# Performance work log

Measured on AMD Instinct MI355X. Metric: run time of the kernel, lower is better.

The kernel has to match this reference:

```python
import jax, jax.numpy as jnp
import numpy as np

NUM_REL = 3


def setup_inputs() -> dict:
    key = jax.random.key(0)
    ks = jax.random.split(key, 12)
    N, E, G = 400_000, 2_000_000, 40_000
    V, D, H, C = 1024, 64, 96, 8
    sc = lambda k, shape: (jax.random.normal(k, shape, jnp.float32) * 0.05)
    return {
        "tokens": jax.random.randint(ks[0], (N,), 0, V),
        "edge_index": jax.random.randint(ks[1], (2, E), 0, N),
        "edge_type": jax.random.randint(ks[2], (E,), 0, NUM_REL),
        "batch": jnp.sort(jax.random.randint(ks[3], (N,), 0, G)),
        "num_graphs": G,
        "emb": sc(ks[4], (V, D)),
        "W1": sc(ks[5], (NUM_REL, D, H)),
        "root1": sc(ks[6], (D, H)),
        "b1": jnp.zeros((H,), jnp.float32),
        "W2": sc(ks[7], (NUM_REL, H, H)),
        "root2": sc(ks[8], (H, H)),
        "b2": jnp.zeros((H,), jnp.float32),
        "linW": sc(ks[9], (H, C)),
        "linb": jnp.zeros((C,), jnp.float32),
    }


def rgcn_layer(x, src, dst, etype, W, root, bias):
    # PyG RGCNConv with default aggr='mean': per-relation mean over incoming
    # edges, transformed by the relation weight, plus root transform and bias.
    N, Din = x.shape
    seg = dst * NUM_REL + etype  # combined (node, relation) segment id
    msgs = x[src]  # [E, Din] irregular gather
    sums = jax.ops.segment_sum(msgs, seg, num_segments=N * NUM_REL)
    sums = sums.reshape(N, NUM_REL, Din)
    cnt = jax.ops.segment_sum(jnp.ones_like(etype, dtype=x.dtype), seg,
                              num_segments=N * NUM_REL).reshape(N, NUM_REL, 1)
    mean = sums / jnp.maximum(cnt, 1.0)
    return jnp.einsum("nrd,rdh->nh", mean, W) + x @ root + bias


def reference(tokens, edge_index, edge_type, batch, num_graphs,
              emb, W1, root1, b1, W2, root2, b2, linW, linb):
    src, dst = edge_index[0], edge_index[1]
    x = emb[tokens]  # [N, D]
    x = jax.nn.relu(rgcn_layer(x, src, dst, edge_type, W1, root1, b1))
    # dropout(p=0.2) is identity in eval mode
    x = jax.nn.relu(rgcn_layer(x, src, dst, edge_type, W2, root2, b2))
    gsum = jax.ops.segment_sum(x, batch, num_segments=num_graphs)
    gcnt = jax.ops.segment_sum(jnp.ones((x.shape[0], 1), x.dtype), batch,
                               num_segments=num_graphs)
    pooled = gsum / jnp.maximum(gcnt, 1.0)  # global_mean_pool
    return pooled @ linW + linb
```

## Files before the change

kernel.cpp:

```cpp
#include <hip/hip_runtime.h>


#define NREL 3
#define DD 64
#define HH 96
#define CC 8
#define TM 16
#define KK 384

typedef __attribute__((ext_vector_type(8))) short bf16x8;
typedef __attribute__((ext_vector_type(4))) short s16x4;
typedef __attribute__((ext_vector_type(4))) float f32x4;

__device__ __forceinline__ unsigned short f2bf(float x) {
    unsigned u = __float_as_uint(x);
    unsigned r = (u + 0x7fffu + ((u >> 16) & 1u)) >> 16;
    return (unsigned short)r;
}
__device__ __forceinline__ float bf2f(unsigned short h) {
    return __uint_as_float(((unsigned)h) << 16);
}

__global__ __launch_bounds__(256) void count_k(const int* __restrict__ dstv,
                                               const int* __restrict__ et, int E,
                                               int* __restrict__ cnt) {
    int e = blockIdx.x * 256 + threadIdx.x;
    if (e < E) atomicAdd(&cnt[dstv[e] * NREL + et[e]], 1);
}

__global__ __launch_bounds__(256) void scan_blk_k(const int* __restrict__ in, int S,
                                                  int* __restrict__ out,
                                                  int* __restrict__ bsum) {
    __shared__ int vals[1024];
    __shared__ int tsum[256];
    int base = blockIdx.x * 1024;
    for (int i = threadIdx.x; i < 1024; i += 256) {
        int g = base + i;
        vals[i] = (g < S) ? in[g] : 0;
    }
    __syncthreads();
    int t = threadIdx.x;
    int a0 = vals[t * 4], a1 = vals[t * 4 + 1], a2 = vals[t * 4 + 2], a3 = vals[t * 4 + 3];
    int s = a0 + a1 + a2 + a3;
    tsum[t] = s;
    __syncthreads();
    for (int off = 1; off < 256; off <<= 1) {
        int v = (t >= off) ? tsum[t - off] : 0;
        __syncthreads();
        tsum[t] += v;
        __syncthreads();
    }
    int excl = tsum[t] - s;
    int g = base + t * 4;
    if (g     < S) out[g]     = excl;
    if (g + 1 < S) out[g + 1] = excl + a0;
    if (g + 2 < S) out[g + 2] = excl + a0 + a1;
    if (g + 3 < S) out[g + 3] = excl + a0 + a1 + a2;
    if (t == 255) bsum[blockIdx.x] = tsum[255];
}

__global__ __launch_bounds__(256) void scan_top_k(int* __restrict__ bsum, int nb) {
    __shared__ int ts[256];
    int t = threadIdx.x;
    int loc[8];
    int s = 0;
    #pragma unroll
    for (int j = 0; j < 8; ++j) {
        int g = t * 8 + j;
        loc[j] = (g < nb) ? bsum[g] : 0;
        s += loc[j];
    }
    ts[t] = s;
    __syncthreads();
    for (int off = 1; off < 256; off <<= 1) {
        int v = (t >= off) ? ts[t - off] : 0;
        __syncthreads();
        ts[t] += v;
        __syncthreads();
    }
    int excl = ts[t] - s;
    #pragma unroll
    for (int j = 0; j < 8; ++j) {
        int g = t * 8 + j;
        if (g < nb) bsum[g] = excl;
        excl += loc[j];
    }
}

__global__ __launch_bounds__(256) void scan_add_k(int* __restrict__ out,
                                                  const int* __restrict__ bsum,
                                                  int S, int E) {
    int i = blockIdx.x * 256 + threadIdx.x;
    if (i < S) out[i] += bsum[i >> 10];
    else if (i == S) out[S] = E;
}

__global__ __launch_bounds__(256) void copy_k(const int* __restrict__ a,
                                              int* __restrict__ b, int n) {
    int i = blockIdx.x * 256 + threadIdx.x;
    if (i < n) b[i] = a[i];
}

__global__ __launch_bounds__(256) void fill_k(const int* __restrict__ srcv,
                                              const int* __restrict__ dstv,
                                              const int* __restrict__ et,
                                              const int* __restrict__ tokens, int E,
                                              int* __restrict__ cursor,
                                              int* __restrict__ ssrc,
                                              int* __restrict__ stok) {
    int e = blockIdx.x * 256 + threadIdx.x;
    if (e >= E) return;
    int s = srcv[e];
    int seg = dstv[e] * NREL + et[e];
    int pos = atomicAdd(&cursor[seg], 1);
    ssrc[pos] = s;
    stok[pos] = tokens[s];
}

__global__ __launch_bounds__(256) void gcnt_k(const int* __restrict__ batch, int N,
                                              float* __restrict__ gcnt) {
    int i = blockIdx.x * 256 + threadIdx.x;
    if (i < N) atomicAdd(&gcnt[batch[i]], 1.0f);
}

__global__ __launch_bounds__(256) void z1er_k(const float* __restrict__ emb,
                                              const float* __restrict__ W1,
                                              const float* __restrict__ root1,
                                              const float* __restrict__ b1,
                                              int V, float* __restrict__ z1,
                                              float* __restrict__ er1) {
    int idx = blockIdx.x * 256 + threadIdx.x;
    int tot = V * 4 * HH;
    if (idx >= tot) return;
    int v = idx / (4 * HH);
    int j = idx - v * 4 * HH;
    int r = j / HH;
    int h = j - r * HH;
    const float* ev = emb + (size_t)v * DD;
    float s = 0.f;
    if (r < NREL) {
        const float* w = W1 + ((size_t)r * DD) * HH + h;
        #pragma unroll 8
        for (int d = 0; d < DD; ++d) s += ev[d] * w[(size_t)d * HH];
        z1[((size_t)v * NREL + r) * HH + h] = s;
    } else {
        const float* w = root1 + h;
        #pragma unroll 8
        for (int d = 0; d < DD; ++d) s += ev[d] * w[(size_t)d * HH];
        er1[(size_t)v * HH + h] = s + b1[h];
    }
}

__global__ __launch_bounds__(256) void catwT_k(const float* __restrict__ W2,
                                               const float* __restrict__ root2,
                                               short* __restrict__ WTh,
                                               short* __restrict__ WTl) {
    int idx = blockIdx.x * 256 + threadIdx.x;
    const int tot = HH * KK;
    if (idx >= tot) return;
    int h = idx / KK;
    int K = idx - h * KK;
    float v = (K < NREL * HH) ? W2[(size_t)K * HH + h]
                              : root2[(size_t)(K - NREL * HH) * HH + h];
    unsigned short hi = f2bf(v);
    float res = v - bf2f(hi);
    unsigned short lo = f2bf(res);
    WTh[(size_t)h * KK + K] = (short)hi;
    WTl[(size_t)h * KK + K] = (short)lo;
}

__global__ __launch_bounds__(256) void l1_k(const int* __restrict__ rowptr,
                                            const int* __restrict__ stok,
                                            const int* __restrict__ tokens,
                                            const float* __restrict__ z1,
                                            const float* __restrict__ er1,
                                            unsigned short* __restrict__ h1h, int N) {
    int idx = blockIdx.x * 256 + threadIdx.x;
    if (idx >= N * 24) return;
    int n = idx / 24;
    int q = idx - n * 24;
    int h0 = q * 4;
    float4 acc = *reinterpret_cast<const float4*>(er1 + (size_t)tokens[n] * HH + h0);
    int base = n * NREL;
    for (int r = 0; r < NREL; ++r) {
        int b = rowptr[base + r], e2 = rowptr[base + r + 1];
        float sx = 0.f, sy = 0.f, sz = 0.f, sw = 0.f;
        for (int i = b; i < e2; i += 4) {
            int m = e2 - i;
            int t0 = stok[i];
            int t1 = stok[i + (m > 1 ? 1 : 0)];
            int t2 = stok[i + (m > 2 ? 2 : 0)];
            int t3 = stok[i + (m > 3 ? 3 : 0)];
            const float4 z0 = *reinterpret_cast<const float4*>(
                z1 + ((size_t)t0 * NREL + r) * HH + h0);
            const float4 zv1 = *reinterpret_cast<const float4*>(
                z1 + ((size_t)t1 * NREL + r) * HH + h0);
            const float4 zv2 = *reinterpret_cast<const float4*>(
                z1 + ((size_t)t2 * NREL + r) * HH + h0);
            const float4 zv3 = *reinterpret_cast<const float4*>(
                z1 + ((size_t)t3 * NREL + r) * HH + h0);
            float w1 = m > 1 ? 1.f : 0.f;
            float w2 = m > 2 ? 1.f : 0.f;
            float w3 = m > 3 ? 1.f : 0.f;
            sx += z0.x + zv1.x * w1 + zv2.x * w2 + zv3.x * w3;
            sy += z0.y + zv1.y * w1 + zv2.y * w2 + zv3.y * w3;
            sz += z0.z + zv1.z * w1 + zv2.z * w2 + zv3.z * w3;
            sw += z0.w + zv1.w * w1 + zv2.w * w2 + zv3.w * w3;
        }
        float rc = 1.0f / fmaxf((float)(e2 - b), 1.0f);
        acc.x += sx * rc; acc.y += sy * rc; acc.z += sz * rc; acc.w += sw * rc;
    }
    s16x4 hv;
    hv[0] = (short)f2bf(fmaxf(acc.x, 0.f));
    hv[1] = (short)f2bf(fmaxf(acc.y, 0.f));
    hv[2] = (short)f2bf(fmaxf(acc.z, 0.f));
    hv[3] = (short)f2bf(fmaxf(acc.w, 0.f));
    *reinterpret_cast<s16x4*>(&h1h[(size_t)n * HH + h0]) = hv;
}

__global__ __launch_bounds__(256) void quant_k(const unsigned short* __restrict__ h1h,
                                               unsigned* __restrict__ h1q, int N) {
    int idx = blockIdx.x * 256 + threadIdx.x;
    int n = idx >> 4;
    int l = idx & 15;
    if (n >= N) return;
    const unsigned* row = reinterpret_cast<const unsigned*>(h1h + (size_t)n * HH) + 3 * l;
    unsigned u0 = row[0], u1 = row[1], u2 = row[2];
    float v[6] = { bf2f((unsigned short)(u0 & 0xffff)), bf2f((unsigned short)(u0 >> 16)),
                   bf2f((unsigned short)(u1 & 0xffff)), bf2f((unsigned short)(u1 >> 16)),
                   bf2f((unsigned short)(u2 & 0xffff)), bf2f((unsigned short)(u2 >> 16)) };
    float m = 0.f;
    #pragma unroll
    for (int j = 0; j < 6; ++j) m = fmaxf(m, v[j]);
    #pragma unroll
    for (int mask = 1; mask <= 8; mask <<= 1) m = fmaxf(m, __shfl_xor(m, mask));
    unsigned eb = __float_as_uint(m) >> 23;
    unsigned E8;
    float qs;
    if (eb < 40) {
        E8 = 0; qs = 0.f;
    } else {
        E8 = eb - 9;
        qs = __uint_as_float((263 - eb) << 23);
    }
    unsigned q[6];
    #pragma unroll
    for (int j = 0; j < 6; ++j) {
        unsigned qi = (unsigned)__float2int_rn(v[j] * qs);
        q[j] = qi > 1023u ? 1023u : qi;
    }
    int d0 = 2 * l;
    unsigned e0 = (E8 >> (2 * (d0 & 3))) & 3u;
    unsigned e1 = (E8 >> (2 * ((d0 + 1) & 3))) & 3u;
    uint2 w;
    w.x = q[0] | (q[1] << 10) | (q[2] << 20) | (e0 << 30);
    w.y = q[3] | (q[4] << 10) | (q[5] << 20) | (e1 << 30);
    *reinterpret_cast<uint2*>(h1q + (size_t)n * 32 + d0) = w;
}

__device__ __forceinline__ float scof(const uint4& c) {
    unsigned E8 = (c.x >> 30) | ((c.y >> 30) << 2) | ((c.z >> 30) << 4)
                | ((c.w >> 30) << 6);
    return __uint_as_float(E8 << 23);
}
__device__ __forceinline__ void dec12(const uint4& c, float sc, float* acc) {
    acc[0]  += (float)(c.x & 1023u) * sc;
    acc[1]  += (float)((c.x >> 10) & 1023u) * sc;
    acc[2]  += (float)((c.x >> 20) & 1023u) * sc;
    acc[3]  += (float)(c.y & 1023u) * sc;
    acc[4]  += (float)((c.y >> 10) & 1023u) * sc;
    acc[5]  += (float)((c.y >> 20) & 1023u) * sc;
    acc[6]  += (float)(c.z & 1023u) * sc;
    acc[7]  += (float)((c.z >> 10) & 1023u) * sc;
    acc[8]  += (float)((c.z >> 20) & 1023u) * sc;
    acc[9]  += (float)(c.w & 1023u) * sc;
    acc[10] += (float)((c.w >> 10) & 1023u) * sc;
    acc[11] += (float)((c.w >> 20) & 1023u) * sc;
}

__global__ __launch_bounds__(384, 7) void l2_k(const int* __restrict__ rowptr,
                                               const int* __restrict__ ssrc,
                                               const unsigned* __restrict__ h1q,
                                               const unsigned short* __restrict__ h1h,
                                               const short* __restrict__ WTh,
                                               const short* __restrict__ WTl,
                                               const float* __restrict__ b2,
                                               const int* __restrict__ batch,
                                               float* __restrict__ gsum, int N) {
    __shared__ float Af32[TM][392];
    __shared__ int rp[49];
    short* ab = (short*)&Af32[0][0];
    int n0 = blockIdx.x * TM;
    int t = threadIdx.x;
    if (t < 49) {
        int idx = n0 * NREL + t;
        int mx = N * NREL;
        rp[t] = rowptr[idx < mx ? idx : mx];
    }
    __syncthreads();
    {
        int grp = t >> 3, l = t & 7;
        int i = grp & 15, r = grp >> 4;
        int n = n0 + i;
        if (n < N) {
            int b = rp[i * NREL + r], e2 = rp[i * NREL + r + 1];
            float acc[12];
            #pragma unroll
            for (int j = 0; j < 12; ++j) acc[j] = 0.f;
            for (int ge = b; ge < e2; ge += 4) {
                int m = e2 - ge;
                int s0 = ssrc[ge];
                int s1 = ssrc[ge + (m > 1 ? 1 : 0)];
                int s2 = ssrc[ge + (m > 2 ? 2 : 0)];
                int s3 = ssrc[ge + (m > 3 ? 3 : 0)];
                uint4 c0 = *reinterpret_cast<const uint4*>(h1q + (size_t)s0 * 32 + 4 * l);
                uint4 c1 = *reinterpret_cast<const uint4*>(h1q + (size_t)s1 * 32 + 4 * l);
                uint4 c2 = *reinterpret_cast<const uint4*>(h1q + (size_t)s2 * 32 + 4 * l);
                uint4 c3 = *reinterpret_cast<const uint4*>(h1q + (size_t)s3 * 32 + 4 * l);
                float f0 = scof(c0);
                float f1 = m > 1 ? scof(c1) : 0.f;
                float f2 = m > 2 ? scof(c2) : 0.f;
                float f3 = m > 3 ? scof(c3) : 0.f;
                dec12(c0, f0, acc);
                dec12(c1, f1, acc);
                dec12(c2, f2, acc);
                dec12(c3, f3, acc);
            }
            float rc = 1.0f / fmaxf((float)(e2 - b), 1.0f);
            #pragma unroll
            for (int j = 0; j < 12; j += 4) {
                float4 v = {acc[j] * rc, acc[j + 1] * rc, acc[j + 2] * rc,
                            acc[j + 3] * rc};
                *reinterpret_cast<float4*>(&Af32[i][r * HH + 12 * l + j]) = v;
            }
        }
    }
    __syncthreads();
    int i2 = t & 15;
    int c2 = t >> 4;
    int d0 = c2 * 16;
    int n2 = n0 + i2;
    float a[16];
    #pragma unroll
    for (int j = 0; j < 16; ++j) a[j] = 0.f;
    if (n2 < N) {
        if (c2 < 18) {
            #pragma unroll
            for (int j = 0; j < 16; ++j) a[j] = Af32[i2][d0 + j];
        } else {
            int k0 = (c2 - 18) * 16;
            const unsigned short* hr = h1h + (size_t)n2 * HH + k0;
            bf16x8 v0 = *reinterpret_cast<const bf16x8*>(hr);
            bf16x8 v1 = *reinterpret_cast<const bf16x8*>(hr + 8);
            #pragma unroll
            for (int j = 0; j < 8; ++j) {
                a[j]     = bf2f((unsigned short)v0[j]);
                a[8 + j] = bf2f((unsigned short)v1[j]);
            }
        }
    }
    __syncthreads();
    {
        bf16x8 hv, lv;
        #pragma unroll
        for (int w = 0; w < 2; ++w) {
            #pragma unroll
            for (int jj = 0; jj < 8; ++jj) {
                float x = a[w * 8 + jj];
                unsigned short hb = f2bf(x);
                float res = x - bf2f(hb);
                hv[jj] = (short)hb;
                lv[jj] = (short)f2bf(res);
            }
            *reinterpret_cast<bf16x8*>(ab + i2 * 392 + d0 + w * 8) = hv;
            *reinterpret_cast<bf16x8*>(ab + TM * 392 + i2 * 392 + d0 + w * 8) = lv;
        }
    }
    __syncthreads();
    int lane = t & 63;
    int w = t >> 6;
    int nb_ = w * 16;
    int r16 = lane & 15;
    int g = lane >> 4;

    float bi = b2[nb_ + r16];
    f32x4 acc = {bi, bi, bi, bi};

    const short* arow_h = ab + r16 * 392 + 8 * g;
    const short* arow_l = ab + TM * 392 + r16 * 392 + 8 * g;
    size_t wb = (size_t)(nb_ + r16) * KK + 8 * g;

    #pragma unroll
    for (int kk = 0; kk < KK / 32; ++kk) {
        int ko = kk * 32;
        bf16x8 ah = *reinterpret_cast<const bf16x8*>(arow_h + ko);
        bf16x8 al = *reinterpret_cast<const bf16x8*>(arow_l + ko);
        bf16x8 bh = *reinterpret_cast<const bf16x8*>(WTh + wb + ko);
        bf16x8 bl = *reinterpret_cast<const bf16x8*>(WTl + wb + ko);
        acc = __builtin_amdgcn_mfma_f32_16x16x32_bf16(ah, bh, acc, 0, 0, 0);
        acc = __builtin_amdgcn_mfma_f32_16x16x32_bf16(al, bh, acc, 0, 0, 0);
        acc = __builtin_amdgcn_mfma_f32_16x16x32_bf16(ah, bl, acc, 0, 0, 0);
    }
    #pragma unroll
    for (int r = 0; r < 4; ++r) {
        int node = n0 + g * 4 + r;
        if (node < N) {
            atomicAdd(gsum + (size_t)batch[node] * HH + nb_ + r16, fmaxf(acc[r], 0.f));
        }
    }
}

__global__ __launch_bounds__(256) void final_k(const float* __restrict__ gsum,
                                               const float* __restrict__ gcnt,
                                               const float* __restrict__ linW,
                                               const float* __restrict__ linb,
                                               float* __restrict__ out, int G) {
    int idx = blockIdx.x * 256 + threadIdx.x;
    if (idx >= G * CC) return;
    int g = idx / CC;
    int c = idx - g * CC;
    float rc = 1.0f / fmaxf(gcnt[g], 1.0f);
    const float* gs = gsum + (size_t)g * HH;
    float s = 0.f;
    #pragma unroll 8
    for (int h = 0; h < HH; ++h) s += gs[h] * linW[h * CC + c];
    out[idx] = s * rc + linb[c];
}

__global__ __launch_bounds__(256) void diag_k(float* __restrict__ out, int n, float v) {
    int i = blockIdx.x * 256 + threadIdx.x;
    if (i < n) out[i] = (i == 0) ? v : 0.f;
}

static inline int nblk(long long n) { return (int)((n + 255) / 256); }

extern "C" void kernel_launch(void* const* d_in, const int* in_sizes, int n_in,
                              void* d_out, int out_size, void* d_ws, size_t ws_size,
                              hipStream_t stream) {
    (void)n_in;
    const int* tokens = (const int*)d_in[0];
    const int* eidx   = (const int*)d_in[1];
    const int* etype  = (const int*)d_in[2];
    const int* batch  = (const int*)d_in[3];
    const float* emb   = (const float*)d_in[5];
    const float* W1    = (const float*)d_in[6];
    const float* root1 = (const float*)d_in[7];
    const float* b1    = (const float*)d_in[8];
    const float* W2    = (const float*)d_in[9];
    const float* root2 = (const float*)d_in[10];
    const float* b2v   = (const float*)d_in[11];
    const float* linW  = (const float*)d_in[12];
    const float* linb  = (const float*)d_in[13];
    float* out = (float*)d_out;

    const int N = in_sizes[0];
    const int E = in_sizes[2];
    const int V = in_sizes[5] / DD;
    const int G = out_size / CC;
    const int S = N * NREL;
    const int nb1 = (S + 1023) / 1024;

    const int* srcv = eidx;
    const int* dstv = eidx + E;

    auto align_up = [](size_t x) { return (x + 255) & ~(size_t)255; };
    size_t o_rowptr = 0;
    size_t o_cnt    = o_rowptr + align_up(((size_t)S + 1) * 4);
    size_t o_bsum   = o_cnt    + align_up((size_t)S * 4);
    size_t o_ssrc   = o_bsum   + align_up((size_t)2048 * 4);
    size_t o_stok   = o_ssrc   + align_up((size_t)E * 4);
    size_t o_z1     = o_stok   + align_up((size_t)E * 4);
    size_t o_er1    = o_z1     + align_up((size_t)V * NREL * HH * 4);
    size_t o_wth    = o_er1    + align_up((size_t)V * HH * 4);
    size_t o_wtl    = o_wth    + align_up((size_t)HH * KK * 2);
    size_t o_gsum   = o_wtl    + align_up((size_t)HH * KK * 2);
    size_t o_gcnt   = o_gsum   + align_up((size_t)G * HH * 4);
    size_t o_h1h    = o_gcnt   + align_up((size_t)G * 4);
    size_t o_h1q    = o_h1h    + align_up((size_t)N * HH * 2);
    size_t need     = o_h1q    + align_up((size_t)N * 128);

    if (ws_size < need || nb1 > 2048) {
        diag_k<<<nblk(out_size), 256, 0, stream>>>(out, out_size, (float)ws_size);
        return;
    }

    char* ws = (char*)d_ws;
    int*   rowptr = (int*)  (ws + o_rowptr);
    int*   cnt    = (int*)  (ws + o_cnt);
    int*   bsum   = (int*)  (ws + o_bsum);
    int*   ssrc   = (int*)  (ws + o_ssrc);
    int*   stok   = (int*)  (ws + o_stok);
    float* z1     = (float*)(ws + o_z1);
    float* er1    = (float*)(ws + o_er1);
    short* WTh    = (short*)(ws + o_wth);
    short* WTl    = (short*)(ws + o_wtl);
    float* gsum   = (float*)(ws + o_gsum);
    float* gcntv  = (float*)(ws + o_gcnt);
    unsigned short* h1h = (unsigned short*)(ws + o_h1h);
    unsigned*       h1q = (unsigned*)(ws + o_h1q);

    hipMemsetAsync(cnt, 0, (size_t)S * 4, stream);
    hipMemsetAsync(gsum, 0, (size_t)G * HH * 4, stream);
    hipMemsetAsync(gcntv, 0, (size_t)G * 4, stream);

    count_k<<<nblk(E), 256, 0, stream>>>(dstv, etype, E, cnt);
    scan_blk_k<<<nb1, 256, 0, stream>>>(cnt, S, rowptr, bsum);
    scan_top_k<<<1, 256, 0, stream>>>(bsum, nb1);
    scan_add_k<<<nblk((long long)S + 1), 256, 0, stream>>>(rowptr, bsum, S, E);
    copy_k<<<nblk(S), 256, 0, stream>>>(rowptr, cnt, S);
    fill_k<<<nblk(E), 256, 0, stream>>>(srcv, dstv, etype, tokens, E, cnt, ssrc, stok);
    z1er_k<<<nblk((long long)V * 4 * HH), 256, 0, stream>>>(emb, W1, root1, b1, V, z1, er1);
    catwT_k<<<nblk(HH * KK), 256, 0, stream>>>(W2, root2, WTh, WTl);
    gcnt_k<<<nblk(N), 256, 0, stream>>>(batch, N, gcntv);
    l1_k<<<nblk((long long)N * 24), 256, 0, stream>>>(rowptr, stok, tokens, z1, er1,
                                                      h1h, N);
    quant_k<<<nblk((long long)N * 16), 256, 0, stream>>>(h1h, h1q, N);
    l2_k<<<(N + TM - 1) / TM, 384, 0, stream>>>(rowptr, ssrc, h1q, h1h, WTh, WTl, b2v,
                                                batch, gsum, N);
    final_k<<<nblk((long long)G * CC), 256, 0, stream>>>(gsum, gcntv, linW, linb, out, G);
}
```

Baseline: 962.5 us.

## Pre-reduce pooled outputs per graph in LDS before atomics; unroll gather by 8

Layer-2 outputs are staged in shared memory, then one thread per feature sums consecutive nodes that share a graph id (batch is sorted) and issues one atomic per run instead of one per node. The edge gather loop now issues eight independent loads per iteration instead of four to expose more memory parallelism. The occupancy hint in launch bounds drops from 7 to 4 to leave room for the extra registers. This cuts global atomic traffic but adds two block barriers and may lower occupancy.

```diff
diff --git a/kernel.cpp b/kernel.cpp
--- a/kernel.cpp
+++ b/kernel.cpp
@@ -278,7 +278,7 @@
     acc[11] += (float)((c.w >> 20) & 1023u) * sc;
 }
 
-__global__ __launch_bounds__(384, 7) void l2_k(const int* __restrict__ rowptr,
+__global__ __launch_bounds__(384, 4) void l2_k(const int* __restrict__ rowptr,
                                                const int* __restrict__ ssrc,
                                                const unsigned* __restrict__ h1q,
                                                const unsigned short* __restrict__ h1h,
@@ -289,6 +289,7 @@
                                                float* __restrict__ gsum, int N) {
     __shared__ float Af32[TM][392];
     __shared__ int rp[49];
+    __shared__ int gb[16];
     short* ab = (short*)&Af32[0][0];
     int n0 = blockIdx.x * TM;
     int t = threadIdx.x;
@@ -296,6 +297,11 @@
         int idx = n0 * NREL + t;
         int mx = N * NREL;
         rp[t] = rowptr[idx < mx ? idx : mx];
+    }
+    if (t >= 64 && t < 80) {
+        int i = t - 64;
+        int n = n0 + i;
+        gb[i] = (n < N) ? batch[n] : -1;
     }
     __syncthreads();
     {
@@ -307,24 +313,32 @@
             float acc[12];
             #pragma unroll
             for (int j = 0; j < 12; ++j) acc[j] = 0.f;
-            for (int ge = b; ge < e2; ge += 4) {
+            for (int ge = b; ge < e2; ge += 8) {
                 int m = e2 - ge;
                 int s0 = ssrc[ge];
                 int s1 = ssrc[ge + (m > 1 ? 1 : 0)];
                 int s2 = ssrc[ge + (m > 2 ? 2 : 0)];
                 int s3 = ssrc[ge + (m > 3 ? 3 : 0)];
+                int s4 = ssrc[ge + (m > 4 ? 4 : 0)];
+                int s5 = ssrc[ge + (m > 5 ? 5 : 0)];
+                int s6 = ssrc[ge + (m > 6 ? 6 : 0)];
+                int s7 = ssrc[ge + (m > 7 ? 7 : 0)];
                 uint4 c0 = *reinterpret_cast<const uint4*>(h1q + (size_t)s0 * 32 + 4 * l);
                 uint4 c1 = *reinterpret_cast<const uint4*>(h1q + (size_t)s1 * 32 + 4 * l);
                 uint4 c2 = *reinterpret_cast<const uint4*>(h1q + (size_t)s2 * 32 + 4 * l);
                 uint4 c3 = *reinterpret_cast<const uint4*>(h1q + (size_t)s3 * 32 + 4 * l);
-                float f0 = scof(c0);
-                float f1 = m > 1 ? scof(c1) : 0.f;
-                float f2 = m > 2 ? scof(c2) : 0.f;
-                float f3 = m > 3 ? scof(c3) : 0.f;
-                dec12(c0, f0, acc);
-                dec12(c1, f1, acc);
-                dec12(c2, f2, acc);
-                dec12(c3, f3, acc);
+                uint4 c4 = *reinterpret_cast<const uint4*>(h1q + (size_t)s4 * 32 + 4 * l);
+                uint4 c5 = *reinterpret_cast<const uint4*>(h1q + (size_t)s5 * 32 + 4 * l);
+                uint4 c6 = *reinterpret_cast<const uint4*>(h1q + (size_t)s6 * 32 + 4 * l);
+                uint4 c7 = *reinterpret_cast<const uint4*>(h1q + (size_t)s7 * 32 + 4 * l);
+                dec12(c0, scof(c0), acc);
+                dec12(c1, m > 1 ? scof(c1) : 0.f, acc);
+                dec12(c2, m > 2 ? scof(c2) : 0.f, acc);
+                dec12(c3, m > 3 ? scof(c3) : 0.f, acc);
+                dec12(c4, m > 4 ? scof(c4) : 0.f, acc);
+                dec12(c5, m > 5 ? scof(c5) : 0.f, acc);
+                dec12(c6, m > 6 ? scof(c6) : 0.f, acc);
+                dec12(c7, m > 7 ? scof(c7) : 0.f, acc);
             }
             float rc = 1.0f / fmaxf((float)(e2 - b), 1.0f);
             #pragma unroll
@@ -401,12 +415,27 @@
         acc = __builtin_amdgcn_mfma_f32_16x16x32_bf16(al, bh, acc, 0, 0, 0);
         acc = __builtin_amdgcn_mfma_f32_16x16x32_bf16(ah, bl, acc, 0, 0, 0);
     }
+    __syncthreads();
+    float* P = (float*)&Af32[0][0];
     #pragma unroll
     for (int r = 0; r < 4; ++r) {
-        int node = n0 + g * 4 + r;
-        if (node < N) {
-            atomicAdd(gsum + (size_t)batch[node] * HH + nb_ + r16, fmaxf(acc[r], 0.f));
+        P[(g * 4 + r) * HH + nb_ + r16] = fmaxf(acc[r], 0.f);
+    }
+    __syncthreads();
+    if (t < HH) {
+        int cur = gb[0];
+        float run = 0.f;
+        #pragma unroll
+        for (int i = 0; i < TM; ++i) {
+            int bg = gb[i];
+            if (bg != cur) {
+                if (cur >= 0) atomicAdd(gsum + (size_t)cur * HH + t, run);
+                run = 0.f;
+                cur = bg;
+            }
+            run += P[i * HH + t];
         }
+        if (cur >= 0) atomicAdd(gsum + (size_t)cur * HH + t, run);
     }
 }
 
```

Result: faster. 924.4 us (-4.0%).
